# Kernel tuning notes

Hardware: AMD Instinct MI355X
Metric: run time of the kernel (lower is better)

The kernel has to match this reference:

```python
import jax, jax.numpy as jnp
import numpy as np

WINDOW = 512
RATIO = 4
NEG = float(jnp.finfo(jnp.bfloat16).min)


def _topk_idxs(S: int, window: int, ratio: int):
    # window indices: for row i, last `window` causal positions, -1 where invalid
    base = jnp.arange(S)[:, None]                      # [S,1]
    w = min(S, window)
    win = jnp.clip(base - window + 1, 0) + jnp.arange(w)  # [S,w]
    win = jnp.where(win > base, -1, win)
    # compressed-KV indices: row i sees first (i+1)//ratio compressed tokens, offset by S
    Sc = S // ratio
    mat = jnp.broadcast_to(jnp.arange(Sc), (S, Sc))    # [S,Sc]
    cmask = mat >= (jnp.arange(1, S + 1)[:, None] // ratio)
    comp = jnp.where(cmask, -1, mat + S)
    return jnp.concatenate([win, comp], axis=-1)       # [S, w+Sc]


def setup_inputs() -> dict:
    key = jax.random.key(0)
    k1, k2, k3, k4 = jax.random.split(key, 4)
    B, S, H, D = 1, 2048, 16, 128
    return {
        "query_states": jax.random.normal(k1, (B, S, H, D), jnp.float32),
        "kv_states": jax.random.normal(k2, (B, S, D), jnp.float32),
        "attn_sink": jax.random.normal(k3, (H,), jnp.float32),
        "kv_compress": jax.random.normal(k4, (B, S // RATIO, D), jnp.float32),
    }


def reference(query_states, kv_states, attn_sink, kv_compress):
    B, S, H, D = query_states.shape
    scale = D ** -0.5
    kv = jnp.concatenate([kv_states, kv_compress], axis=1)  # [B, KV, D]
    KV = kv.shape[1]
    q = jnp.transpose(query_states, (0, 2, 1, 3))            # [B, H, S, D]
    attn = jnp.einsum('bhsd,bkd->bhsk', q, kv) * scale       # [B, H, S, KV]
    # additive mask from topk indices; -1 wraps to padding column KV, then trimmed
    idxs = _topk_idxs(S, WINDOW, RATIO)                       # [S, K]
    mask = jnp.full((S, KV + 1), NEG, dtype=attn.dtype)
    mask = mask.at[jnp.arange(S)[:, None], idxs].set(0.0)[:, :-1]  # [S, KV]
    attn = attn + mask[None, None]
    sinks = jnp.broadcast_to(attn_sink.reshape(1, H, 1, 1), (B, H, S, 1))
    logits = jnp.concatenate([attn, sinks], axis=-1)          # [B, H, S, KV+1]
    probs = jax.nn.softmax(logits, axis=-1)
    scores = probs[..., :-1]
    out = jnp.einsum('bhsk,bkd->bhsd', scores, kv)
    return jnp.transpose(out, (0, 2, 1, 3))                   # [B, S, H, D]
```

## Files before the change

### kernel.cpp

```cpp
#include <hip/hip_runtime.h>


typedef __attribute__((ext_vector_type(8))) short bf16x8;
typedef __attribute__((ext_vector_type(4))) float f32x4;
typedef unsigned short u16;
typedef unsigned int u32;

constexpr int S = 2048, H = 16, D = 128, WIN = 512;
constexpr int QB = 4, HG = 8;
constexpr int NT = 256;
constexpr int KVROWS = 2592;

__device__ __forceinline__ u16 f2bf(float f) {
  u32 u = __builtin_bit_cast(u32, f);
  return (u16)((u + 0x7FFFu + ((u >> 16) & 1u)) >> 16);
}

__global__ __launch_bounds__(256) void precvt_kv(
    const float* __restrict__ kvs, const float* __restrict__ kvc,
    u16* __restrict__ dst) {
  int idx = blockIdx.x * 256 + threadIdx.x;
  if (idx >= KVROWS * (D / 8)) return;
  int row = idx >> 4, c8 = (idx & 15) * 8;
  float4 a = make_float4(0.f, 0.f, 0.f, 0.f), b = a;
  if (row < 2048) {
    const float4* p = (const float4*)(kvs + (size_t)row * D + c8);
    a = p[0]; b = p[1];
  } else if (row < 2560) {
    const float4* p = (const float4*)(kvc + (size_t)(row - 2048) * D + c8);
    a = p[0]; b = p[1];
  }
  bf16x8 v;
  v[0] = (short)f2bf(a.x); v[1] = (short)f2bf(a.y);
  v[2] = (short)f2bf(a.z); v[3] = (short)f2bf(a.w);
  v[4] = (short)f2bf(b.x); v[5] = (short)f2bf(b.y);
  v[6] = (short)f2bf(b.z); v[7] = (short)f2bf(b.w);
  *(bf16x8*)(dst + (size_t)row * D + c8) = v;
}

__global__ __launch_bounds__(NT, 3) void sparse_attn_mfma3(
    const float* __restrict__ q, const u16* __restrict__ kvb,
    const float* __restrict__ sink, float* __restrict__ out) {

  const int it = (int)(gridDim.x - 1u - blockIdx.x);
  const int i0 = it * QB;
  const int h0 = blockIdx.y * HG;
  const int tid = threadIdx.x;
  const int wave = tid >> 6, lane = tid & 63;
  const int split = wave >> 1, mtg = wave & 1;
  const int lm = lane & 15, lg = lane >> 4;

  __shared__ __align__(16) char smem[41984];
  u16 (*Ksub)[8][4][16] = (u16(*)[8][4][16])(smem + split * 8192);
  u16 (*KTl)[40]        = (u16(*)[40])(smem + 16384 + split * 10240);
  u16 (*Pll)[40]        = (u16(*)[40])(smem + 36864 + wave * 1280);

  const int iq = i0 + (lm & 3);
  const int hh = h0 + mtg * 4 + (lm >> 2);

  const float qscale = 0.08838834764831845f;
  bf16x8 qf[4];
  {
    const float* qp = q + ((size_t)iq * H + hh) * D;
#pragma unroll
    for (int kt = 0; kt < 4; ++kt) {
      const float4* p4 = (const float4*)(qp + kt * 32 + lg * 8);
      float4 a = p4[0], b = p4[1];
      bf16x8 v;
      v[0] = (short)f2bf(a.x * qscale); v[1] = (short)f2bf(a.y * qscale);
      v[2] = (short)f2bf(a.z * qscale); v[3] = (short)f2bf(a.w * qscale);
      v[4] = (short)f2bf(b.x * qscale); v[5] = (short)f2bf(b.y * qscale);
      v[6] = (short)f2bf(b.z * qscale); v[7] = (short)f2bf(b.w * qscale);
      qf[kt] = v;
    }
  }

  const float sk = sink[hh];
  float m_run = sk, l_run = 0.f;
  f32x4 oacc[8];
  const f32x4 fzero = {0.f, 0.f, 0.f, 0.f};
#pragma unroll
  for (int b = 0; b < 8; ++b) oacc[b] = fzero;

  const int w_lo = (i0 > WIN - 1) ? (i0 - (WIN - 1)) : 0;
  const int n1r = i0 + QB - w_lo;
  const int n2r = (i0 + QB) >> 2;
  const int nt1 = (n1r + 31) >> 5;
  const int nt2 = (n2r + 31) >> 5;
  const int ntiles = nt1 + nt2;
  const int kmax = (ntiles + 1) >> 1;

  const int st = tid & 127;
  const int st_t7 = st & 7, st_r0 = st_t7 * 4, st_dc = st >> 3;

  uint4 sreg[4];
  auto sload = [&](int tt) {
    const int row0 = (tt < nt1) ? (w_lo + tt * 32) : (2048 + (tt - nt1) * 32);
    const u16* p = kvb + (size_t)(row0 + st_r0) * D + st_dc * 8;
#pragma unroll
    for (int rr = 0; rr < 4; ++rr)
      sreg[rr] = *(const uint4*)(p + (size_t)rr * D);
  };

  auto swrite = [&]() {
#pragma unroll
    for (int rr = 0; rr < 4; ++rr) {
      int rowp = rr ^ (st_t7 & 3);
      *(uint4*)&Ksub[st_t7][st_dc >> 1][rowp][(st_dc & 1) * 8] = sreg[rr];
    }
    const u32* R0 = (const u32*)&sreg[0];
    const u32* R1 = (const u32*)&sreg[1];
    const u32* R2 = (const u32*)&sreg[2];
    const u32* R3 = (const u32*)&sreg[3];
#pragma unroll
    for (int dd2 = 0; dd2 < 4; ++dd2) {
#pragma unroll
      for (int h = 0; h < 2; ++h) {
        const u32 sel = h ? 0x07060302u : 0x05040100u;
        u32 lo = __builtin_amdgcn_perm(R1[dd2], R0[dd2], sel);
        u32 hi = __builtin_amdgcn_perm(R3[dd2], R2[dd2], sel);
        int dl = st_dc * 8 + dd2 * 2 + h;
        int dphys = (dl & ~7) | ((dl & 7) ^ (st_dc & 7));
        *(uint2*)&KTl[dphys][st_r0] = make_uint2(lo, hi);
      }
    }
  };

  sload(split);

  const int rrA = (lm & 3) ^ ((lm >> 2) & 3);

  for (int k = 0; k < kmax; ++k) {
    const int tt = 2 * k + split;
    const bool active = tt < ntiles;
    __syncthreads();
    if (active) swrite();
    __syncthreads();
    const int tn = tt + 2;
    if (tn < ntiles) sload(tn);
    if (!active) continue;

    const bool isw = tt < nt1;
    const int row0 = isw ? (w_lo + tt * 32) : ((tt - nt1) * 32);

    f32x4 tacc[2];
    tacc[0] = fzero; tacc[1] = fzero;
    __builtin_amdgcn_s_setprio(1);
#pragma unroll
    for (int kt = 0; kt < 4; ++kt) {
      const int ds = kt * 2 + (lg >> 1), co = (lg & 1) * 8;
      bf16x8 a0 = *(const bf16x8*)&Ksub[(lm >> 2)][ds][rrA][co];
      bf16x8 a1 = *(const bf16x8*)&Ksub[4 + (lm >> 2)][ds][rrA][co];
      tacc[0] = __builtin_amdgcn_mfma_f32_16x16x32_bf16(a0, qf[kt], tacc[0], 0, 0, 0);
      tacc[1] = __builtin_amdgcn_mfma_f32_16x16x32_bf16(a1, qf[kt], tacc[1], 0, 0, 0);
    }
    __builtin_amdgcn_s_setprio(0);

    float vv[8];
    float tm = -1e30f;
    const bool fullv = isw ? (row0 >= i0 + 3 - (WIN - 1)) && (row0 + 31 <= i0)
                           : ((row0 + 31) * 4 + 3 <= i0);
    if (fullv) {
#pragma unroll
      for (int k2 = 0; k2 < 2; ++k2)
#pragma unroll
        for (int r = 0; r < 4; ++r) {
          float x = tacc[k2][r];
          vv[k2 * 4 + r] = x;
          tm = fmaxf(tm, x);
        }
    } else {
#pragma unroll
      for (int k2 = 0; k2 < 2; ++k2)
#pragma unroll
        for (int r = 0; r < 4; ++r) {
          int jj = row0 + k2 * 16 + lg * 4 + r;
          float x = tacc[k2][r];
          bool ok = isw ? (jj <= iq && jj + WIN > iq) : (jj * 4 + 3 <= iq);
          x = ok ? x : -1e30f;
          vv[k2 * 4 + r] = x;
          tm = fmaxf(tm, x);
        }
    }
    tm = fmaxf(tm, __shfl_xor(tm, 16));
    tm = fmaxf(tm, __shfl_xor(tm, 32));
    if (__any(tm > m_run + 8.f)) {
      float mn = fmaxf(m_run, tm);
      float fs = __expf(m_run - mn);
      m_run = mn; l_run *= fs;
#pragma unroll
      for (int dt = 0; dt < 8; ++dt) oacc[dt] *= fs;
    }
    float s = 0.f;
#pragma unroll
    for (int k2 = 0; k2 < 2; ++k2) {
      u16 pb[4];
#pragma unroll
      for (int r = 0; r < 4; ++r) {
        float p = __expf(vv[k2 * 4 + r] - m_run);
        s += p; pb[r] = f2bf(p);
      }
      *(uint2*)&Pll[lm][k2 * 16 + lg * 4] =
          make_uint2((u32)pb[0] | ((u32)pb[1] << 16),
                     (u32)pb[2] | ((u32)pb[3] << 16));
    }
    l_run += s;

    bf16x8 pf = *(const bf16x8*)&Pll[lm][lg * 8];
    __builtin_amdgcn_s_setprio(1);
#pragma unroll
    for (int dt = 0; dt < 8; ++dt) {
      int d = dt * 16 + lm;
      int drow = (d & ~7) | ((d & 7) ^ ((d >> 3) & 7));
      bf16x8 vf = *(const bf16x8*)&KTl[drow][lg * 8];
      oacc[dt] = __builtin_amdgcn_mfma_f32_16x16x32_bf16(vf, pf, oacc[dt], 0, 0, 0);
    }
    __builtin_amdgcn_s_setprio(0);
  }

  float l = l_run;
  l += __shfl_xor(l, 16);
  l += __shfl_xor(l, 32);

  float (*Ocomb)[16][128] = (float(*)[16][128])(smem);
  float* Mcomb = (float*)(smem + 16384);
  float* Lcomb = (float*)(smem + 16384 + 128);

  __syncthreads();
  if (split == 1) {
#pragma unroll
    for (int dt = 0; dt < 8; ++dt)
      *(f32x4*)&Ocomb[mtg][lm][dt * 16 + lg * 4] = oacc[dt];
    if (lg == 0) { Mcomb[mtg * 16 + lm] = m_run; Lcomb[mtg * 16 + lm] = l; }
  }
  __syncthreads();
  if (split == 0) {
    float m1 = Mcomb[mtg * 16 + lm], l1 = Lcomb[mtg * 16 + lm];
    float mf = fmaxf(m_run, m1);
    float a0 = __expf(m_run - mf), a1 = __expf(m1 - mf);
    float lf = l * a0 + l1 * a1 + __expf(sk - mf);
    float di = 1.f / lf;
    float* op = out + ((size_t)iq * H + hh) * D;
#pragma unroll
    for (int dt = 0; dt < 8; ++dt) {
      f32x4 o1 = *(f32x4*)&Ocomb[mtg][lm][dt * 16 + lg * 4];
      float4 w4 = make_float4((oacc[dt][0] * a0 + o1[0] * a1) * di,
                              (oacc[dt][1] * a0 + o1[1] * a1) * di,
                              (oacc[dt][2] * a0 + o1[2] * a1) * di,
                              (oacc[dt][3] * a0 + o1[3] * a1) * di);
      *(float4*)(op + dt * 16 + lg * 4) = w4;
    }
  }
}

extern "C" void kernel_launch(void* const* d_in, const int* in_sizes, int n_in,
                              void* d_out, int out_size, void* d_ws, size_t ws_size,
                              hipStream_t stream) {
  const float* q    = (const float*)d_in[0];
  const float* kvs  = (const float*)d_in[1];
  const float* sink = (const float*)d_in[2];
  const float* kvc  = (const float*)d_in[3];
  float* out = (float*)d_out;
  u16* kvb = (u16*)d_ws;

  {
    int nthr = KVROWS * (D / 8);
    precvt_kv<<<(nthr + 255) / 256, 256, 0, stream>>>(kvs, kvc, kvb);
  }
  dim3 grid(S / QB, H / HG);
  sparse_attn_mfma3<<<grid, NT, 0, stream>>>(q, kvb, sink, out);
}
```

Measured before the change: 117.1 us.

## Double query rows per block and use 64-row KV tiles without split-K

Each block now handles 8 query rows instead of 4, and each wave covers 8 rows times 2 heads. The two-way KV split across wave pairs, along with its shared-memory combine step, is removed; all four waves walk every 64-row KV tile together. This aims to halve redundant KV loads per query, double MFMA work per barrier and drop the final reduction. In exchange the grid has half as many blocks, each with a longer serial tile loop, and there are more masked elements in boundary tiles.

```diff
diff --git a/kernel.cpp b/kernel.cpp
--- a/kernel.cpp
+++ b/kernel.cpp
@@ -7,8 +7,9 @@
 typedef unsigned int u32;
 
 constexpr int S = 2048, H = 16, D = 128, WIN = 512;
-constexpr int QB = 4, HG = 8;
+constexpr int QB = 8, HG = 8;
 constexpr int NT = 256;
+constexpr int KVB = 64;
 constexpr int KVROWS = 2592;
 
 __device__ __forceinline__ u16 f2bf(float f) {
@@ -38,7 +39,7 @@
   *(bf16x8*)(dst + (size_t)row * D + c8) = v;
 }
 
-__global__ __launch_bounds__(NT, 3) void sparse_attn_mfma3(
+__global__ __launch_bounds__(NT, 3) void sparse_attn_mfma8(
     const float* __restrict__ q, const u16* __restrict__ kvb,
     const float* __restrict__ sink, float* __restrict__ out) {
 
@@ -47,16 +48,15 @@
   const int h0 = blockIdx.y * HG;
   const int tid = threadIdx.x;
   const int wave = tid >> 6, lane = tid & 63;
-  const int split = wave >> 1, mtg = wave & 1;
   const int lm = lane & 15, lg = lane >> 4;
 
-  __shared__ __align__(16) char smem[41984];
-  u16 (*Ksub)[8][4][16] = (u16(*)[8][4][16])(smem + split * 8192);
-  u16 (*KTl)[40]        = (u16(*)[40])(smem + 16384 + split * 10240);
-  u16 (*Pll)[40]        = (u16(*)[40])(smem + 36864 + wave * 1280);
-
-  const int iq = i0 + (lm & 3);
-  const int hh = h0 + mtg * 4 + (lm >> 2);
+  __shared__ __align__(16) u16 Ksub[16][8][4][16];
+  __shared__ __align__(16) u16 KTl[128][72];
+  __shared__ __align__(16) u16 Pll4[4][16][72];
+  u16 (*Pll)[72] = Pll4[wave];
+
+  const int iq = i0 + (lm & 7);
+  const int hh = h0 + wave * 2 + (lm >> 3);
 
   const float qscale = 0.08838834764831845f;
   bf16x8 qf[4];
@@ -85,17 +85,17 @@
   const int w_lo = (i0 > WIN - 1) ? (i0 - (WIN - 1)) : 0;
   const int n1r = i0 + QB - w_lo;
   const int n2r = (i0 + QB) >> 2;
-  const int nt1 = (n1r + 31) >> 5;
-  const int nt2 = (n2r + 31) >> 5;
+  const int nt1 = (n1r + KVB - 1) >> 6;
+  const int nt2 = (n2r + KVB - 1) >> 6;
   const int ntiles = nt1 + nt2;
-  const int kmax = (ntiles + 1) >> 1;
-
-  const int st = tid & 127;
-  const int st_t7 = st & 7, st_r0 = st_t7 * 4, st_dc = st >> 3;
+
+  const int st_dc = tid & 15;
+  const int st_t  = tid >> 4;
+  const int st_r0 = st_t * 4;
 
   uint4 sreg[4];
   auto sload = [&](int tt) {
-    const int row0 = (tt < nt1) ? (w_lo + tt * 32) : (2048 + (tt - nt1) * 32);
+    const int row0 = (tt < nt1) ? (w_lo + tt * KVB) : (2048 + (tt - nt1) * KVB);
     const u16* p = kvb + (size_t)(row0 + st_r0) * D + st_dc * 8;
 #pragma unroll
     for (int rr = 0; rr < 4; ++rr)
@@ -105,8 +105,8 @@
   auto swrite = [&]() {
 #pragma unroll
     for (int rr = 0; rr < 4; ++rr) {
-      int rowp = rr ^ (st_t7 & 3);
-      *(uint4*)&Ksub[st_t7][st_dc >> 1][rowp][(st_dc & 1) * 8] = sreg[rr];
+      int rowp = rr ^ (st_t & 3);
+      *(uint4*)&Ksub[st_t][st_dc >> 1][rowp][(st_dc & 1) * 8] = sreg[rr];
     }
     const u32* R0 = (const u32*)&sreg[0];
     const u32* R1 = (const u32*)&sreg[1];
@@ -126,59 +126,56 @@
     }
   };
 
-  sload(split);
+  sload(0);
 
   const int rrA = (lm & 3) ^ ((lm >> 2) & 3);
 
-  for (int k = 0; k < kmax; ++k) {
-    const int tt = 2 * k + split;
-    const bool active = tt < ntiles;
+  for (int t = 0; t < ntiles; ++t) {
     __syncthreads();
-    if (active) swrite();
+    swrite();
     __syncthreads();
-    const int tn = tt + 2;
-    if (tn < ntiles) sload(tn);
-    if (!active) continue;
-
-    const bool isw = tt < nt1;
-    const int row0 = isw ? (w_lo + tt * 32) : ((tt - nt1) * 32);
-
-    f32x4 tacc[2];
-    tacc[0] = fzero; tacc[1] = fzero;
+    if (t + 1 < ntiles) sload(t + 1);
+
+    const bool isw = t < nt1;
+    const int row0 = isw ? (w_lo + t * KVB) : ((t - nt1) * KVB);
+
+    f32x4 tacc[4];
+    tacc[0] = fzero; tacc[1] = fzero; tacc[2] = fzero; tacc[3] = fzero;
     __builtin_amdgcn_s_setprio(1);
 #pragma unroll
     for (int kt = 0; kt < 4; ++kt) {
       const int ds = kt * 2 + (lg >> 1), co = (lg & 1) * 8;
-      bf16x8 a0 = *(const bf16x8*)&Ksub[(lm >> 2)][ds][rrA][co];
-      bf16x8 a1 = *(const bf16x8*)&Ksub[4 + (lm >> 2)][ds][rrA][co];
-      tacc[0] = __builtin_amdgcn_mfma_f32_16x16x32_bf16(a0, qf[kt], tacc[0], 0, 0, 0);
-      tacc[1] = __builtin_amdgcn_mfma_f32_16x16x32_bf16(a1, qf[kt], tacc[1], 0, 0, 0);
+#pragma unroll
+      for (int k4 = 0; k4 < 4; ++k4) {
+        bf16x8 a = *(const bf16x8*)&Ksub[k4 * 4 + (lm >> 2)][ds][rrA][co];
+        tacc[k4] = __builtin_amdgcn_mfma_f32_16x16x32_bf16(a, qf[kt], tacc[k4], 0, 0, 0);
+      }
     }
     __builtin_amdgcn_s_setprio(0);
 
-    float vv[8];
+    float vv[16];
     float tm = -1e30f;
-    const bool fullv = isw ? (row0 >= i0 + 3 - (WIN - 1)) && (row0 + 31 <= i0)
-                           : ((row0 + 31) * 4 + 3 <= i0);
+    const bool fullv = isw ? (row0 >= i0 + (QB - 1) - (WIN - 1)) && (row0 + KVB - 1 <= i0)
+                           : ((row0 + KVB - 1) * 4 + 3 <= i0);
     if (fullv) {
 #pragma unroll
-      for (int k2 = 0; k2 < 2; ++k2)
+      for (int k4 = 0; k4 < 4; ++k4)
 #pragma unroll
         for (int r = 0; r < 4; ++r) {
-          float x = tacc[k2][r];
-          vv[k2 * 4 + r] = x;
+          float x = tacc[k4][r];
+          vv[k4 * 4 + r] = x;
           tm = fmaxf(tm, x);
         }
     } else {
 #pragma unroll
-      for (int k2 = 0; k2 < 2; ++k2)
+      for (int k4 = 0; k4 < 4; ++k4)
 #pragma unroll
         for (int r = 0; r < 4; ++r) {
-          int jj = row0 + k2 * 16 + lg * 4 + r;
-          float x = tacc[k2][r];
+          int jj = row0 + k4 * 16 + lg * 4 + r;
+          float x = tacc[k4][r];
           bool ok = isw ? (jj <= iq && jj + WIN > iq) : (jj * 4 + 3 <= iq);
           x = ok ? x : -1e30f;
-          vv[k2 * 4 + r] = x;
+          vv[k4 * 4 + r] = x;
           tm = fmaxf(tm, x);
         }
     }
@@ -193,27 +190,30 @@
     }
     float s = 0.f;
 #pragma unroll
-    for (int k2 = 0; k2 < 2; ++k2) {
+    for (int k4 = 0; k4 < 4; ++k4) {
       u16 pb[4];
 #pragma unroll
       for (int r = 0; r < 4; ++r) {
-        float p = __expf(vv[k2 * 4 + r] - m_run);
+        float p = __expf(vv[k4 * 4 + r] - m_run);
         s += p; pb[r] = f2bf(p);
       }
-      *(uint2*)&Pll[lm][k2 * 16 + lg * 4] =
+      *(uint2*)&Pll[lm][k4 * 16 + lg * 4] =
           make_uint2((u32)pb[0] | ((u32)pb[1] << 16),
                      (u32)pb[2] | ((u32)pb[3] << 16));
     }
     l_run += s;
 
-    bf16x8 pf = *(const bf16x8*)&Pll[lm][lg * 8];
+    bf16x8 pf0 = *(const bf16x8*)&Pll[lm][lg * 8];
+    bf16x8 pf1 = *(const bf16x8*)&Pll[lm][32 + lg * 8];
     __builtin_amdgcn_s_setprio(1);
 #pragma unroll
     for (int dt = 0; dt < 8; ++dt) {
       int d = dt * 16 + lm;
       int drow = (d & ~7) | ((d & 7) ^ ((d >> 3) & 7));
-      bf16x8 vf = *(const bf16x8*)&KTl[drow][lg * 8];
-      oacc[dt] = __builtin_amdgcn_mfma_f32_16x16x32_bf16(vf, pf, oacc[dt], 0, 0, 0);
+      bf16x8 vf0 = *(const bf16x8*)&KTl[drow][lg * 8];
+      bf16x8 vf1 = *(const bf16x8*)&KTl[drow][32 + lg * 8];
+      oacc[dt] = __builtin_amdgcn_mfma_f32_16x16x32_bf16(vf0, pf0, oacc[dt], 0, 0, 0);
+      oacc[dt] = __builtin_amdgcn_mfma_f32_16x16x32_bf16(vf1, pf1, oacc[dt], 0, 0, 0);
     }
     __builtin_amdgcn_s_setprio(0);
   }
@@ -221,35 +221,14 @@
   float l = l_run;
   l += __shfl_xor(l, 16);
   l += __shfl_xor(l, 32);
-
-  float (*Ocomb)[16][128] = (float(*)[16][128])(smem);
-  float* Mcomb = (float*)(smem + 16384);
-  float* Lcomb = (float*)(smem + 16384 + 128);
-
-  __syncthreads();
-  if (split == 1) {
-#pragma unroll
-    for (int dt = 0; dt < 8; ++dt)
-      *(f32x4*)&Ocomb[mtg][lm][dt * 16 + lg * 4] = oacc[dt];
-    if (lg == 0) { Mcomb[mtg * 16 + lm] = m_run; Lcomb[mtg * 16 + lm] = l; }
-  }
-  __syncthreads();
-  if (split == 0) {
-    float m1 = Mcomb[mtg * 16 + lm], l1 = Lcomb[mtg * 16 + lm];
-    float mf = fmaxf(m_run, m1);
-    float a0 = __expf(m_run - mf), a1 = __expf(m1 - mf);
-    float lf = l * a0 + l1 * a1 + __expf(sk - mf);
-    float di = 1.f / lf;
-    float* op = out + ((size_t)iq * H + hh) * D;
-#pragma unroll
-    for (int dt = 0; dt < 8; ++dt) {
-      f32x4 o1 = *(f32x4*)&Ocomb[mtg][lm][dt * 16 + lg * 4];
-      float4 w4 = make_float4((oacc[dt][0] * a0 + o1[0] * a1) * di,
-                              (oacc[dt][1] * a0 + o1[1] * a1) * di,
-                              (oacc[dt][2] * a0 + o1[2] * a1) * di,
-                              (oacc[dt][3] * a0 + o1[3] * a1) * di);
-      *(float4*)(op + dt * 16 + lg * 4) = w4;
-    }
+  l += __expf(sk - m_run);
+  float di = 1.f / l;
+  float* op = out + ((size_t)iq * H + hh) * D;
+#pragma unroll
+  for (int dt = 0; dt < 8; ++dt) {
+    f32x4 o = oacc[dt];
+    float4 w4 = make_float4(o[0] * di, o[1] * di, o[2] * di, o[3] * di);
+    *(float4*)(op + dt * 16 + lg * 4) = w4;
   }
 }
 
@@ -268,5 +247,5 @@
     precvt_kv<<<(nthr + 255) / 256, 256, 0, stream>>>(kvs, kvc, kvb);
   }
   dim3 grid(S / QB, H / HG);
-  sparse_attn_mfma3<<<grid, NT, 0, stream>>>(q, kvb, sink, out);
-}
+  sparse_attn_mfma8<<<grid, NT, 0, stream>>>(q, kvb, sink, out);
+}
```

After: 111.7 us. 4.6% less time.
